# Optimization experiments

Measured on AMD Instinct MI355X. Metric: run time of the kernel, lower is better.

Reference implementation:

```python
import jax, jax.numpy as jnp
import numpy as np


def pfaffian(A):
    """Pfaffian of even-dim skew-symmetric A via Parlett-Reid LTL^T (no pivoting).
    pf(A) = prod over elimination steps of the (k, k+1) pivot."""
    n = A.shape[0]
    ar = jnp.arange(n)

    def step(carry, i):
        A, pf = carry
        k = 2 * i
        pivot = A[k, k + 1]
        mask = ar > (k + 1)                      # rows/cols k+2:
        tau = jnp.where(mask, A[k, :], 0.0) / pivot
        col = jnp.where(mask, A[:, k + 1], 0.0)
        # rank-2 skew update of the trailing submatrix
        A = A + tau[:, None] * col[None, :] - col[:, None] * tau[None, :]
        return (A, pf * pivot), None

    (A, pf), _ = jax.lax.scan(step, (A, jnp.ones((), A.dtype)), jnp.arange(n // 2))
    return pf


def setup_inputs() -> dict:
    key = jax.random.key(0)
    k1, k2 = jax.random.split(key)
    N = 128          # nsites; Nparticle = N (spin system, one particle per site)
    B = 128          # batch of Monte-Carlo configurations
    x = jax.random.normal(k1, (B, N), jnp.float32)
    scale = np.float32(np.sqrt(np.e / N))
    F = jax.random.normal(k2, (N * (2 * N - 1),), jnp.float32) * scale
    return {"x": x, "F": F}


def reference(x, F):
    N = x.shape[-1]
    Nparticle = N
    twoN = 2 * N
    # scatter parameter vector into strict lower triangle, antisymmetrize
    F_full = jnp.zeros((twoN, twoN), F.dtype).at[jnp.tril_indices(twoN, -1)].set(F)
    F_full = F_full - F_full.T

    def single(xi):
        # spin system: up orbitals where x>0, down orbitals where x<=0
        occ = jnp.concatenate([xi > 0, xi <= 0])
        idx = jnp.flatnonzero(occ, size=Nparticle)
        A = F_full[idx[:, None], idx[None, :]]   # [Nparticle, Nparticle] gather
        return pfaffian(A)

    return jax.vmap(single)(x)
```

## Files before the change

kernel.cpp:

```cpp
#include <hip/hip_runtime.h>


#define RL(v, l) __int_as_float(__builtin_amdgcn_readlane(__float_as_int(v), (l)))

__global__ __launch_bounds__(512) void pfaffian_kernel(
    const float* __restrict__ x,
    const float* __restrict__ F,
    float* __restrict__ out)
{
    const int b    = blockIdx.x;
    const int t    = threadIdx.x;
    const int lane = t & 63;
    const int wave = t >> 6;

    __shared__ int idx_sh[128];
    __shared__ int wtot[4];
    __shared__ __align__(16) float tauLDS[4][128];
    __shared__ __align__(16) float colLDS[4][128];
    __shared__ __align__(16) float rS[4][128];
    __shared__ __align__(16) float cS[4][128];

    if (t < 256) {
        const float xv  = x[b * 128 + (t & 127)];
        const bool  pos = xv > 0.0f;
        const bool  o   = (t < 128) ? pos : !pos;
        const unsigned long long mm = __ballot(o);
        const int rank = __popcll(mm & ((1ull << lane) - 1ull));
        if (lane == 63) wtot[wave] = rank + (o ? 1 : 0);
        __syncthreads();
        int off = 0;
#pragma unroll
        for (int w = 0; w < 4; ++w)
            if (w < wave) off += wtot[w];
        if (o) idx_sh[off + rank] = t;
    } else {
        __syncthreads();
    }
    __syncthreads();

    const int rg   = t >> 4;
    const int cg   = t & 15;
    const int row0 = rg << 2;
    const int col0 = cg << 3;

    int ri[4], ci[8];
#pragma unroll
    for (int a = 0; a < 4; ++a) ri[a] = idx_sh[row0 + a];
#pragma unroll
    for (int c = 0; c < 8; ++c) ci[c] = idx_sh[col0 + c];

    float A[4][8];
#pragma unroll
    for (int a = 0; a < 4; ++a) {
        const int ii = ri[a];
#pragma unroll
        for (int c = 0; c < 8; ++c) {
            const int jj = ci[c];
            const int hi = ii > jj ? ii : jj;
            const int lo = ii > jj ? jj : ii;
            float v = (ii == jj) ? 0.0f : F[(hi * (hi - 1)) / 2 + lo];
            A[a][c] = (ii < jj) ? -v : v;
        }
    }

    auto stage_next = [&](int rgbase, int cgbase) {
        if (rg == rgbase) {
            *(float4*)&rS[0][col0]     = make_float4(A[0][0], A[0][1], A[0][2], A[0][3]);
            *(float4*)&rS[0][col0 + 4] = make_float4(A[0][4], A[0][5], A[0][6], A[0][7]);
            *(float4*)&rS[1][col0]     = make_float4(A[2][0], A[2][1], A[2][2], A[2][3]);
            *(float4*)&rS[1][col0 + 4] = make_float4(A[2][4], A[2][5], A[2][6], A[2][7]);
        }
        if (rg == rgbase + 1) {
            *(float4*)&rS[2][col0]     = make_float4(A[0][0], A[0][1], A[0][2], A[0][3]);
            *(float4*)&rS[2][col0 + 4] = make_float4(A[0][4], A[0][5], A[0][6], A[0][7]);
            *(float4*)&rS[3][col0]     = make_float4(A[2][0], A[2][1], A[2][2], A[2][3]);
            *(float4*)&rS[3][col0 + 4] = make_float4(A[2][4], A[2][5], A[2][6], A[2][7]);
        }
        if (cg == cgbase) {
            *(float4*)&cS[0][row0] = make_float4(A[0][1], A[1][1], A[2][1], A[3][1]);
            *(float4*)&cS[1][row0] = make_float4(A[0][3], A[1][3], A[2][3], A[3][3]);
            *(float4*)&cS[2][row0] = make_float4(A[0][5], A[1][5], A[2][5], A[3][5]);
            *(float4*)&cS[3][row0] = make_float4(A[0][7], A[1][7], A[2][7], A[3][7]);
        }
    };
    stage_next(0, 0);

    float pf = 1.0f;
    for (int P = 0; P < 16; ++P) {
        __syncthreads();

        if (wave == 0) {
            const int g0 = lane << 1;
            const int g1 = g0 + 1;
            float R[4][2], C[4][2], TAU[4][2], CV[4][2];
#pragma unroll
            for (int j = 0; j < 4; ++j) {
                const float2 rv = *(const float2*)&rS[j][g0];
                const float2 cv = *(const float2*)&cS[j][g0];
                R[j][0] = rv.x; R[j][1] = rv.y;
                C[j][0] = cv.x; C[j][1] = cv.y;
            }
#pragma unroll
            for (int j = 0; j < 4; ++j) {
                const int k = 8 * P + 2 * j;
                const float piv = RL(R[j][1], 4 * P + j);
                pf = __fmul_rn(pf, piv);

                TAU[j][0] = (g0 > k + 1) ? __fdiv_rn(R[j][0], piv) : 0.0f;
                TAU[j][1] = (g1 > k + 1) ? __fdiv_rn(R[j][1], piv) : 0.0f;
                CV[j][0]  = (g0 > k + 1) ? C[j][0] : 0.0f;
                CV[j][1]  = (g1 > k + 1) ? C[j][1] : 0.0f;

                *(float2*)&tauLDS[j][g0] = make_float2(TAU[j][0], TAU[j][1]);
                *(float2*)&colLDS[j][g0] = make_float2(CV[j][0], CV[j][1]);

#pragma unroll
                for (int j2 = j + 1; j2 < 4; ++j2) {
                    const int ls = 4 * P + j2;
                    const float tau_r = RL(TAU[j][0], ls);
                    const float col_r = RL(CV[j][0], ls);
                    R[j2][0] = __fmaf_rn(-col_r, TAU[j][0],
                               __fmaf_rn(tau_r, CV[j][0], R[j2][0]));
                    R[j2][1] = __fmaf_rn(-col_r, TAU[j][1],
                               __fmaf_rn(tau_r, CV[j][1], R[j2][1]));
                    const float tau_c = RL(TAU[j][1], ls);
                    const float col_c = RL(CV[j][1], ls);
                    C[j2][0] = __fmaf_rn(-CV[j][0], tau_c,
                               __fmaf_rn(TAU[j][0], col_c, C[j2][0]));
                    C[j2][1] = __fmaf_rn(-CV[j][1], tau_c,
                               __fmaf_rn(TAU[j][1], col_c, C[j2][1]));
                }
            }
        }
        __syncthreads();

        if (2 * wave + 1 > P) {
#pragma unroll
            for (int j = 0; j < 4; ++j) {
                const float4 trv = *(const float4*)&tauLDS[j][row0];
                const float4 crv = *(const float4*)&colLDS[j][row0];
                const float4 t0v = *(const float4*)&tauLDS[j][col0];
                const float4 t1v = *(const float4*)&tauLDS[j][col0 + 4];
                const float4 c0v = *(const float4*)&colLDS[j][col0];
                const float4 c1v = *(const float4*)&colLDS[j][col0 + 4];
                const float tr[4] = {trv.x, trv.y, trv.z, trv.w};
                const float cr[4] = {crv.x, crv.y, crv.z, crv.w};
                const float tc[8] = {t0v.x, t0v.y, t0v.z, t0v.w,
                                     t1v.x, t1v.y, t1v.z, t1v.w};
                const float cc[8] = {c0v.x, c0v.y, c0v.z, c0v.w,
                                     c1v.x, c1v.y, c1v.z, c1v.w};
#pragma unroll
                for (int a = 0; a < 4; ++a) {
#pragma unroll
                    for (int c = 0; c < 8; ++c) {
                        A[a][c] = __fmaf_rn(-cr[a], tc[c],
                                  __fmaf_rn(tr[a], cc[c], A[a][c]));
                    }
                }
            }
            if (P < 15) stage_next(2 * P + 2, P + 1);
        }
    }

    if (t == 0) out[b] = pf;
}

extern "C" void kernel_launch(void* const* d_in, const int* in_sizes, int n_in,
                              void* d_out, int out_size, void* d_ws, size_t ws_size,
                              hipStream_t stream) {
    const float* x = (const float*)d_in[0];
    const float* F = (const float*)d_in[1];
    float* out     = (float*)d_out;
    (void)in_sizes; (void)n_in; (void)out_size; (void)d_ws; (void)ws_size;

    pfaffian_kernel<<<128, 512, 0, stream>>>(x, F, out);
}
```

Before: 79.52 us.

## Pipeline panel factorization one step ahead with dedicated wave and double-buffered LDS

Wave 0 becomes a dedicated panel worker. It factors panel P+1, applying the previous panel's rank-2 updates to the staged rows and columns itself, while waves 1-7 apply panel P's trailing update. LDS staging and the tau/col buffers are double-buffered, so each panel step now needs one barrier instead of two and the serial panel work overlaps the bulk update. In exchange, wave 0 no longer updates its own tile rows, the stages are staged two panels ahead, and LDS use doubles.

```diff
diff --git a/kernel.cpp b/kernel.cpp
--- a/kernel.cpp
+++ b/kernel.cpp
@@ -15,10 +15,10 @@
 
     __shared__ int idx_sh[128];
     __shared__ int wtot[4];
-    __shared__ __align__(16) float tauLDS[4][128];
-    __shared__ __align__(16) float colLDS[4][128];
-    __shared__ __align__(16) float rS[4][128];
-    __shared__ __align__(16) float cS[4][128];
+    __shared__ __align__(16) float tauLDS[2][4][128];
+    __shared__ __align__(16) float colLDS[2][4][128];
+    __shared__ __align__(16) float rS[2][4][128];
+    __shared__ __align__(16) float cS[2][4][128];
 
     if (t < 256) {
         const float xv  = x[b * 128 + (t & 127)];
@@ -63,86 +63,117 @@
         }
     }
 
-    auto stage_next = [&](int rgbase, int cgbase) {
+    auto stage = [&](int Pn, int st) {
+        const int rgbase = 2 * Pn;
         if (rg == rgbase) {
-            *(float4*)&rS[0][col0]     = make_float4(A[0][0], A[0][1], A[0][2], A[0][3]);
-            *(float4*)&rS[0][col0 + 4] = make_float4(A[0][4], A[0][5], A[0][6], A[0][7]);
-            *(float4*)&rS[1][col0]     = make_float4(A[2][0], A[2][1], A[2][2], A[2][3]);
-            *(float4*)&rS[1][col0 + 4] = make_float4(A[2][4], A[2][5], A[2][6], A[2][7]);
+            *(float4*)&rS[st][0][col0]     = make_float4(A[0][0], A[0][1], A[0][2], A[0][3]);
+            *(float4*)&rS[st][0][col0 + 4] = make_float4(A[0][4], A[0][5], A[0][6], A[0][7]);
+            *(float4*)&rS[st][1][col0]     = make_float4(A[2][0], A[2][1], A[2][2], A[2][3]);
+            *(float4*)&rS[st][1][col0 + 4] = make_float4(A[2][4], A[2][5], A[2][6], A[2][7]);
         }
         if (rg == rgbase + 1) {
-            *(float4*)&rS[2][col0]     = make_float4(A[0][0], A[0][1], A[0][2], A[0][3]);
-            *(float4*)&rS[2][col0 + 4] = make_float4(A[0][4], A[0][5], A[0][6], A[0][7]);
-            *(float4*)&rS[3][col0]     = make_float4(A[2][0], A[2][1], A[2][2], A[2][3]);
-            *(float4*)&rS[3][col0 + 4] = make_float4(A[2][4], A[2][5], A[2][6], A[2][7]);
-        }
-        if (cg == cgbase) {
-            *(float4*)&cS[0][row0] = make_float4(A[0][1], A[1][1], A[2][1], A[3][1]);
-            *(float4*)&cS[1][row0] = make_float4(A[0][3], A[1][3], A[2][3], A[3][3]);
-            *(float4*)&cS[2][row0] = make_float4(A[0][5], A[1][5], A[2][5], A[3][5]);
-            *(float4*)&cS[3][row0] = make_float4(A[0][7], A[1][7], A[2][7], A[3][7]);
+            *(float4*)&rS[st][2][col0]     = make_float4(A[0][0], A[0][1], A[0][2], A[0][3]);
+            *(float4*)&rS[st][2][col0 + 4] = make_float4(A[0][4], A[0][5], A[0][6], A[0][7]);
+            *(float4*)&rS[st][3][col0]     = make_float4(A[2][0], A[2][1], A[2][2], A[2][3]);
+            *(float4*)&rS[st][3][col0 + 4] = make_float4(A[2][4], A[2][5], A[2][6], A[2][7]);
+        }
+        if (cg == Pn) {
+            *(float4*)&cS[st][0][row0] = make_float4(A[0][1], A[1][1], A[2][1], A[3][1]);
+            *(float4*)&cS[st][1][row0] = make_float4(A[0][3], A[1][3], A[2][3], A[3][3]);
+            *(float4*)&cS[st][2][row0] = make_float4(A[0][5], A[1][5], A[2][5], A[3][5]);
+            *(float4*)&cS[st][3][row0] = make_float4(A[0][7], A[1][7], A[2][7], A[3][7]);
         }
     };
-    stage_next(0, 0);
+    stage(0, 0);
+    stage(1, 1);
+    __syncthreads();
 
     float pf = 1.0f;
-    for (int P = 0; P < 16; ++P) {
-        __syncthreads();
-
-        if (wave == 0) {
-            const int g0 = lane << 1;
-            const int g1 = g0 + 1;
-            float R[4][2], C[4][2], TAU[4][2], CV[4][2];
-#pragma unroll
-            for (int j = 0; j < 4; ++j) {
-                const float2 rv = *(const float2*)&rS[j][g0];
-                const float2 cv = *(const float2*)&cS[j][g0];
-                R[j][0] = rv.x; R[j][1] = rv.y;
-                C[j][0] = cv.x; C[j][1] = cv.y;
-            }
-#pragma unroll
-            for (int j = 0; j < 4; ++j) {
-                const int k = 8 * P + 2 * j;
-                const float piv = RL(R[j][1], 4 * P + j);
-                pf = __fmul_rn(pf, piv);
-
-                TAU[j][0] = (g0 > k + 1) ? __fdiv_rn(R[j][0], piv) : 0.0f;
-                TAU[j][1] = (g1 > k + 1) ? __fdiv_rn(R[j][1], piv) : 0.0f;
-                CV[j][0]  = (g0 > k + 1) ? C[j][0] : 0.0f;
-                CV[j][1]  = (g1 > k + 1) ? C[j][1] : 0.0f;
-
-                *(float2*)&tauLDS[j][g0] = make_float2(TAU[j][0], TAU[j][1]);
-                *(float2*)&colLDS[j][g0] = make_float2(CV[j][0], CV[j][1]);
-
-#pragma unroll
-                for (int j2 = j + 1; j2 < 4; ++j2) {
-                    const int ls = 4 * P + j2;
-                    const float tau_r = RL(TAU[j][0], ls);
-                    const float col_r = RL(CV[j][0], ls);
-                    R[j2][0] = __fmaf_rn(-col_r, TAU[j][0],
-                               __fmaf_rn(tau_r, CV[j][0], R[j2][0]));
-                    R[j2][1] = __fmaf_rn(-col_r, TAU[j][1],
-                               __fmaf_rn(tau_r, CV[j][1], R[j2][1]));
-                    const float tau_c = RL(TAU[j][1], ls);
-                    const float col_c = RL(CV[j][1], ls);
-                    C[j2][0] = __fmaf_rn(-CV[j][0], tau_c,
-                               __fmaf_rn(TAU[j][0], col_c, C[j2][0]));
-                    C[j2][1] = __fmaf_rn(-CV[j][1], tau_c,
-                               __fmaf_rn(TAU[j][1], col_c, C[j2][1]));
+    float TAUp[4][2], CVp[4][2];
+
+    auto crew = [&](int Pn, bool pre) {
+        const int sv = Pn & 1;
+        const int g0 = lane << 1;
+        const int g1 = g0 + 1;
+        float R[4][2], C[4][2];
+#pragma unroll
+        for (int j = 0; j < 4; ++j) {
+            const float2 rv = *(const float2*)&rS[sv][j][g0];
+            const float2 cv = *(const float2*)&cS[sv][j][g0];
+            R[j][0] = rv.x; R[j][1] = rv.y;
+            C[j][0] = cv.x; C[j][1] = cv.y;
+        }
+        if (pre) {
+#pragma unroll
+            for (int jp = 0; jp < 4; ++jp) {
+#pragma unroll
+                for (int a = 0; a < 4; ++a) {
+                    const int la = 4 * Pn + a;
+                    const float tau_r = RL(TAUp[jp][0], la);
+                    const float col_r = RL(CVp[jp][0], la);
+                    R[a][0] = __fmaf_rn(-col_r, TAUp[jp][0],
+                              __fmaf_rn(tau_r, CVp[jp][0], R[a][0]));
+                    R[a][1] = __fmaf_rn(-col_r, TAUp[jp][1],
+                              __fmaf_rn(tau_r, CVp[jp][1], R[a][1]));
+                    const float tau_c = RL(TAUp[jp][1], la);
+                    const float col_c = RL(CVp[jp][1], la);
+                    C[a][0] = __fmaf_rn(-CVp[jp][0], tau_c,
+                              __fmaf_rn(TAUp[jp][0], col_c, C[a][0]));
+                    C[a][1] = __fmaf_rn(-CVp[jp][1], tau_c,
+                              __fmaf_rn(TAUp[jp][1], col_c, C[a][1]));
                 }
             }
         }
-        __syncthreads();
-
-        if (2 * wave + 1 > P) {
+        float TAU[4][2], CV[4][2];
+#pragma unroll
+        for (int j = 0; j < 4; ++j) {
+            const int k = 8 * Pn + 2 * j;
+            const float piv = RL(R[j][1], 4 * Pn + j);
+            pf = __fmul_rn(pf, piv);
+            TAU[j][0] = (g0 > k + 1) ? __fdiv_rn(R[j][0], piv) : 0.0f;
+            TAU[j][1] = (g1 > k + 1) ? __fdiv_rn(R[j][1], piv) : 0.0f;
+            CV[j][0]  = (g0 > k + 1) ? C[j][0] : 0.0f;
+            CV[j][1]  = (g1 > k + 1) ? C[j][1] : 0.0f;
+            *(float2*)&tauLDS[sv][j][g0] = make_float2(TAU[j][0], TAU[j][1]);
+            *(float2*)&colLDS[sv][j][g0] = make_float2(CV[j][0], CV[j][1]);
+#pragma unroll
+            for (int j2 = j + 1; j2 < 4; ++j2) {
+                const int ls = 4 * Pn + j2;
+                const float tau_r = RL(TAU[j][0], ls);
+                const float col_r = RL(CV[j][0], ls);
+                R[j2][0] = __fmaf_rn(-col_r, TAU[j][0],
+                           __fmaf_rn(tau_r, CV[j][0], R[j2][0]));
+                R[j2][1] = __fmaf_rn(-col_r, TAU[j][1],
+                           __fmaf_rn(tau_r, CV[j][1], R[j2][1]));
+                const float tau_c = RL(TAU[j][1], ls);
+                const float col_c = RL(CV[j][1], ls);
+                C[j2][0] = __fmaf_rn(-CV[j][0], tau_c,
+                           __fmaf_rn(TAU[j][0], col_c, C[j2][0]));
+                C[j2][1] = __fmaf_rn(-CV[j][1], tau_c,
+                           __fmaf_rn(TAU[j][1], col_c, C[j2][1]));
+            }
+        }
+#pragma unroll
+        for (int j = 0; j < 4; ++j) {
+            TAUp[j][0] = TAU[j][0]; TAUp[j][1] = TAU[j][1];
+            CVp[j][0]  = CV[j][0];  CVp[j][1]  = CV[j][1];
+        }
+    };
+
+    if (wave == 0) crew(0, false);
+    __syncthreads();
+
+    for (int P = 0; P < 15; ++P) {
+        if (wave >= 1 && 2 * wave > P) {
+            const int sp = P & 1;
 #pragma unroll
             for (int j = 0; j < 4; ++j) {
-                const float4 trv = *(const float4*)&tauLDS[j][row0];
-                const float4 crv = *(const float4*)&colLDS[j][row0];
-                const float4 t0v = *(const float4*)&tauLDS[j][col0];
-                const float4 t1v = *(const float4*)&tauLDS[j][col0 + 4];
-                const float4 c0v = *(const float4*)&colLDS[j][col0];
-                const float4 c1v = *(const float4*)&colLDS[j][col0 + 4];
+                const float4 trv = *(const float4*)&tauLDS[sp][j][row0];
+                const float4 crv = *(const float4*)&colLDS[sp][j][row0];
+                const float4 t0v = *(const float4*)&tauLDS[sp][j][col0];
+                const float4 t1v = *(const float4*)&tauLDS[sp][j][col0 + 4];
+                const float4 c0v = *(const float4*)&colLDS[sp][j][col0];
+                const float4 c1v = *(const float4*)&colLDS[sp][j][col0 + 4];
                 const float tr[4] = {trv.x, trv.y, trv.z, trv.w};
                 const float cr[4] = {crv.x, crv.y, crv.z, crv.w};
                 const float tc[8] = {t0v.x, t0v.y, t0v.z, t0v.w,
@@ -158,8 +189,10 @@
                     }
                 }
             }
-            if (P < 15) stage_next(2 * P + 2, P + 1);
-        }
+            if (P <= 13) stage(P + 2, P & 1);
+        }
+        if (wave == 0) crew(P + 1, true);
+        __syncthreads();
     }
 
     if (t == 0) out[b] = pf;
```

New measurement: 76.10 us. 1.04x faster.
